# Kernel tuning notes

Hardware: AMD Instinct MI355X
Metric: run time of the kernel (lower is better)

## Reference

```python
import jax, jax.numpy as jnp
import numpy as np

N_ACTIVE = 32

def setup_inputs() -> dict:
    key = jax.random.key(0)
    ks = jax.random.split(key, 6)
    B, T, D, G, GD = 4, 2048, 2048, 4096, 256
    x = jax.random.normal(ks[0], (B, T, D), jnp.float32)
    Wc = jax.random.normal(ks[1], (G, D), jnp.float32) * (D ** -0.5)   # context_proj weight
    temperature = jnp.array(1.0, jnp.float32)
    genes = jax.random.normal(ks[2], (G, GD), jnp.float32) * 0.02      # dna_bank gene table
    Wd = jax.random.normal(ks[3], (D, GD), jnp.float32) * (GD ** -0.5) # gene_to_down weight
    Wu = jax.random.normal(ks[4], (D, GD), jnp.float32) * 0.02         # gene_to_up (zeros in init; random for testing)
    norm_w = jnp.ones((D,), jnp.float32)                               # RMSNorm weight
    scale = jnp.array(0.1, jnp.float32)
    return {"x": x, "Wc": Wc, "temperature": temperature, "genes": genes,
            "Wd": Wd, "Wu": Wu, "norm_w": norm_w, "scale": scale}

def reference(x, Wc, temperature, genes, Wd, Wu, norm_w, scale):
    # RMSNorm (torch default eps = finfo(dtype).eps, learnable elementwise weight)
    eps = jnp.finfo(x.dtype).eps
    xn = x * jax.lax.rsqrt(jnp.mean(x * x, axis=-1, keepdims=True) + eps) * norm_w
    # Expression: router logits over gene bank, temperature clamped at 0.1
    logits = jnp.einsum('btd,gd->btg', xn, Wc) / jnp.clip(temperature, 0.1)
    # top-k + scatter(-inf) + softmax == softmax over top-k values, zeros elsewhere
    top_vals, top_idx = jax.lax.top_k(logits, N_ACTIVE)        # (B,T,K)
    expr_w = jax.nn.softmax(top_vals, axis=-1)                 # (B,T,K)
    # dna_bank.express: weighted combination of genes. Only top-k entries are
    # nonzero, so gather + weighted sum is mathematically identical to the
    # dense (B,T,G)@(G,GD) combine the original materializes.
    expressed = jnp.einsum('btk,btkc->btc', expr_w, genes[top_idx])  # (B,T,GD)
    down = jnp.tanh(jnp.einsum('btc,dc->btd', expressed, Wd))
    up = jnp.einsum('btc,dc->btd', expressed, Wu)
    return down * xn * up * scale
```

## Files before the change

### kernel.cpp

```cpp
#include <hip/hip_runtime.h>
#include <math.h>

#define M_TOK 8192
#define D_DIM 2048
#define G_GENES 4096
#define GD_DIM 256
#define KSEL 32
#define NCAND 40
#define NSLICE 8

typedef float f32x4 __attribute__((ext_vector_type(4)));
typedef short bf16x8 __attribute__((ext_vector_type(8)));

__device__ __forceinline__ void async_copy16(const void* g, void* lds) {
  __builtin_amdgcn_global_load_lds((const __attribute__((address_space(1))) void*)g,
                                   (__attribute__((address_space(3))) void*)lds, 16, 0, 0);
}

__device__ __forceinline__ unsigned short f2bf(float f) {
  unsigned int u = __float_as_uint(f);
  unsigned int r = (u + 0x7fffu + ((u >> 16) & 1u)) >> 16;
  return (unsigned short)r;
}
__device__ __forceinline__ float bf2f(unsigned short h) {
  return __uint_as_float(((unsigned int)h) << 16);
}

__global__ __launch_bounds__(256) void k1_rmsnorm(const float* __restrict__ x,
                                                  const float* __restrict__ nw,
                                                  float* __restrict__ r_out,
                                                  unsigned short* __restrict__ xn_bf) {
  int t = blockIdx.x, tid = threadIdx.x;
  const float4* xr = (const float4*)(x + (size_t)t * D_DIM);
  float4 a = xr[tid], b = xr[tid + 256];
  double ss = (double)a.x*a.x + (double)a.y*a.y + (double)a.z*a.z + (double)a.w*a.w
            + (double)b.x*b.x + (double)b.y*b.y + (double)b.z*b.z + (double)b.w*b.w;
  for (int off = 32; off; off >>= 1) ss += __shfl_down(ss, off);
  __shared__ double sred[4];
  __shared__ float rshare;
  int lane = tid & 63, wv = tid >> 6;
  if (lane == 0) sred[wv] = ss;
  __syncthreads();
  if (tid == 0) {
    double tot = sred[0] + sred[1] + sred[2] + sred[3];
    float r = (float)(1.0 / sqrt(tot / (double)D_DIM + 1.1920928955078125e-7));
    rshare = r; r_out[t] = r;
  }
  __syncthreads();
  float r = rshare;
  const float4* nw4 = (const float4*)nw;
  float4 na = nw4[tid], nb = nw4[tid + 256];
  ushort4 oa, ob;
  oa.x = f2bf(a.x * r * na.x); oa.y = f2bf(a.y * r * na.y);
  oa.z = f2bf(a.z * r * na.z); oa.w = f2bf(a.w * r * na.w);
  ob.x = f2bf(b.x * r * nb.x); ob.y = f2bf(b.y * r * nb.y);
  ob.z = f2bf(b.z * r * nb.z); ob.w = f2bf(b.w * r * nb.w);
  ushort4* o4 = (ushort4*)(xn_bf + (size_t)t * D_DIM);
  o4[tid] = oa; o4[tid + 256] = ob;
}

__global__ __launch_bounds__(256) void k2_cvt(const float* __restrict__ w,
                                              unsigned short* __restrict__ wb) {
  size_t i = (size_t)blockIdx.x * 256 + threadIdx.x;
  const float4* w4 = (const float4*)w;
  float4 a = w4[2*i], b = w4[2*i+1];
  ushort4 oa, ob;
  oa.x = f2bf(a.x); oa.y = f2bf(a.y); oa.z = f2bf(a.z); oa.w = f2bf(a.w);
  ob.x = f2bf(b.x); ob.y = f2bf(b.y); ob.z = f2bf(b.z); ob.w = f2bf(b.w);
  ((ushort4*)wb)[2*i] = oa; ((ushort4*)wb)[2*i+1] = ob;
}

__global__ __launch_bounds__(256) void k2b_split(const float* __restrict__ wd,
                                                 const float* __restrict__ wu,
                                                 unsigned short* __restrict__ wdh,
                                                 unsigned short* __restrict__ wdl,
                                                 unsigned short* __restrict__ wuh,
                                                 unsigned short* __restrict__ wul) {
  const float* src = blockIdx.y ? wu : wd;
  unsigned short* dh = blockIdx.y ? wuh : wdh;
  unsigned short* dl = blockIdx.y ? wul : wdl;
  size_t i = (size_t)blockIdx.x * 256 + threadIdx.x;
  float4 v = ((const float4*)src)[i];
  ushort4 h, l;
  h.x = f2bf(v.x); l.x = f2bf(v.x - bf2f(h.x));
  h.y = f2bf(v.y); l.y = f2bf(v.y - bf2f(h.y));
  h.z = f2bf(v.z); l.z = f2bf(v.z - bf2f(h.z));
  h.w = f2bf(v.w); l.w = f2bf(v.w - bf2f(h.w));
  ((ushort4*)dh)[i] = h;
  ((ushort4*)dl)[i] = l;
}

__global__ __launch_bounds__(512, 1) void k3_gemm_logits(const unsigned short* __restrict__ A,
                                                         const unsigned short* __restrict__ B,
                                                         unsigned short* __restrict__ C) {
  __shared__ unsigned short As[4][256 * 32];
  __shared__ unsigned short Bs[4][256 * 32];
  const int tid = threadIdx.x;
  const int lane = tid & 63, wv = tid >> 6;
  const int wm = wv >> 2, wn = wv & 3;
  int lin = blockIdx.x;
  int swz = (lin & 7) * 64 + (lin >> 3);
  const int bm = swz & 31, bn = swz >> 5;

  const int grow = lane >> 2;
  const int gslot = (lane & 3) ^ ((lane >> 3) & 3);
  const unsigned short* agp = A + (size_t)(bm * 256 + wv * 32 + grow) * D_DIM + gslot * 8;
  const unsigned short* bgp = B + (size_t)(bn * 256 + wv * 32 + grow) * D_DIM + gslot * 8;
  const int fr = lane & 15;
  const int sw8 = (((lane >> 4) ^ ((lane >> 1) & 3))) * 8;

  f32x4 acc[8][4];
#pragma unroll
  for (int m = 0; m < 8; ++m)
#pragma unroll
    for (int n = 0; n < 4; ++n) acc[m][n] = (f32x4){0.f, 0.f, 0.f, 0.f};

#define STAGE_A3(t_) { const int b_ = (t_) & 3; const int kt_ = (t_) * 32;          \
    async_copy16(agp + kt_,              &As[b_][(wv * 32) * 32]);                   \
    async_copy16(agp + kt_ + 16 * D_DIM, &As[b_][(wv * 32 + 16) * 32]); }
#define STAGE_B3(t_) { const int b_ = (t_) & 3; const int kt_ = (t_) * 32;          \
    async_copy16(bgp + kt_,              &Bs[b_][(wv * 32) * 32]);                   \
    async_copy16(bgp + kt_ + 16 * D_DIM, &Bs[b_][(wv * 32 + 16) * 32]); }

  STAGE_A3(0); STAGE_B3(0);
  STAGE_A3(1); STAGE_B3(1);
  STAGE_A3(2); STAGE_B3(2);
  asm volatile("s_waitcnt vmcnt(8)" ::: "memory");
  __builtin_amdgcn_s_barrier();

#pragma unroll 1
  for (int t = 0; t < 64; ++t) {
    const int c = t & 3;
    const unsigned short* as = As[c];
    const unsigned short* bs = Bs[c];
    bf16x8 fa[4], fb[4];
#pragma unroll
    for (int n = 0; n < 4; ++n)
      fb[n] = *(const bf16x8*)&bs[(wn * 64 + n * 16 + fr) * 32 + sw8];
#pragma unroll
    for (int m = 0; m < 4; ++m)
      fa[m] = *(const bf16x8*)&as[(wm * 128 + m * 16 + fr) * 32 + sw8];
    if (t + 3 < 64) STAGE_A3(t + 3);
    __builtin_amdgcn_s_barrier();
    asm volatile("s_waitcnt lgkmcnt(0)" ::: "memory");
    __builtin_amdgcn_sched_barrier(0);
    __builtin_amdgcn_s_setprio(1);
#pragma unroll
    for (int m = 0; m < 4; ++m)
#pragma unroll
      for (int n = 0; n < 4; ++n)
        acc[m][n] = __builtin_amdgcn_mfma_f32_16x16x32_bf16(fa[m], fb[n], acc[m][n], 0, 0, 0);
    __builtin_amdgcn_s_setprio(0);
    __builtin_amdgcn_s_barrier();
#pragma unroll
    for (int m = 0; m < 4; ++m)
      fa[m] = *(const bf16x8*)&as[(wm * 128 + 64 + m * 16 + fr) * 32 + sw8];
    if (t + 3 < 64) STAGE_B3(t + 3);
    __builtin_amdgcn_s_barrier();
    asm volatile("s_waitcnt lgkmcnt(0)" ::: "memory");
    __builtin_amdgcn_sched_barrier(0);
    __builtin_amdgcn_s_setprio(1);
#pragma unroll
    for (int m = 0; m < 4; ++m)
#pragma unroll
      for (int n = 0; n < 4; ++n)
        acc[m + 4][n] = __builtin_amdgcn_mfma_f32_16x16x32_bf16(fa[m], fb[n], acc[m + 4][n], 0, 0, 0);
    __builtin_amdgcn_s_setprio(0);
    if (t <= 60)      { asm volatile("s_waitcnt vmcnt(8)" ::: "memory"); }
    else if (t == 61) { asm volatile("s_waitcnt vmcnt(4)" ::: "memory"); }
    else if (t == 62) { asm volatile("s_waitcnt vmcnt(0)" ::: "memory"); }
    __builtin_amdgcn_s_barrier();
  }
#undef STAGE_A3
#undef STAGE_B3

#pragma unroll
  for (int m = 0; m < 8; ++m)
#pragma unroll
    for (int n = 0; n < 4; ++n)
#pragma unroll
      for (int j = 0; j < 4; ++j) {
        int row = bm * 256 + wm * 128 + m * 16 + (lane >> 4) * 4 + j;
        int col = bn * 256 + wn * 64 + n * 16 + fr;
        C[(size_t)row * G_GENES + col] = f2bf(acc[m][n][j]);
      }
}

__global__ __launch_bounds__(256) void k4_topk(const unsigned short* __restrict__ L,
                                               int* __restrict__ cand) {
  int wv = threadIdx.x >> 6, lane = threadIdx.x & 63;
  int t = blockIdx.x * 4 + wv;
  const unsigned short* lp = L + (size_t)t * G_GENES;
  unsigned kp[32];
#pragma unroll
  for (int i = 0; i < 8; ++i) {
    uint4 raw = *(const uint4*)(lp + i * 512 + lane * 8);
    unsigned rr[4] = {raw.x, raw.y, raw.z, raw.w};
#pragma unroll
    for (int q = 0; q < 4; ++q) {
      unsigned r = rr[q];
      unsigned s = (r >> 15) & 0x00010001u;
      unsigned xm = 0x80008000u | (s * 0x7FFFu);
      kp[i * 4 + q] = r ^ xm;
    }
  }
  unsigned lo = 0, hi = 65536;
  while (hi - lo > 1u) {
    unsigned mid = (lo + hi) >> 1;
    int c = 0;
#pragma unroll
    for (int q = 0; q < 32; ++q) {
      c += __popcll(__ballot((kp[q] & 0xFFFFu) >= mid));
      c += __popcll(__ballot((kp[q] >> 16) >= mid));
    }
    if (c >= NCAND) lo = mid; else hi = mid;
  }
  const unsigned T = lo;
  unsigned long long below = (1ull << lane) - 1ull;
  int* outp = cand + (size_t)t * NCAND;
  int cnt = 0;
#pragma unroll
  for (int q = 0; q < 32; ++q) {
#pragma unroll
    for (int h = 0; h < 2; ++h) {
      unsigned key = h ? (kp[q] >> 16) : (kp[q] & 0xFFFFu);
      bool pred = key > T;
      unsigned long long m = __ballot(pred);
      if (pred) {
        int pos = cnt + (int)__popcll(m & below);
        outp[pos] = (q >> 2) * 512 + lane * 8 + (q & 3) * 2 + h;
      }
      cnt += (int)__popcll(m);
    }
  }
#pragma unroll 1
  for (int q = 0; q < 32 && cnt < NCAND; ++q) {
#pragma unroll
    for (int h = 0; h < 2; ++h) {
      unsigned key = h ? (kp[q] >> 16) : (kp[q] & 0xFFFFu);
      bool pred = key == T;
      unsigned long long m = __ballot(pred);
      if (pred) {
        int pos = cnt + (int)__popcll(m & below);
        if (pos < NCAND)
          outp[pos] = (q >> 2) * 512 + lane * 8 + (q & 3) * 2 + h;
      }
      cnt += (int)__popcll(m);
    }
  }
}

__global__ __launch_bounds__(256) void k5a_partial(const float* __restrict__ x,
                                                   const float* __restrict__ r,
                                                   const float* __restrict__ nw,
                                                   const float* __restrict__ Wc,
                                                   const int* __restrict__ cand,
                                                   double* __restrict__ part) {
  int bid = blockIdx.x;
  int slice = bid & 7;
  int group = bid >> 3;
  int wv = threadIdx.x >> 6, lane = threadIdx.x & 63;
  const int dbase = slice * 256;
  float4 nv = *(const float4*)(nw + dbase + lane * 4);
  bool b0 = (lane & 1) != 0, b1 = (lane & 2) != 0, b2 = (lane & 4) != 0;
#pragma unroll 1
  for (int tt = 0; tt < 2; ++tt) {
    int t = group * 8 + wv * 2 + tt;
    float rr = r[t];
    float4 xv = *(const float4*)(x + (size_t)t * D_DIM + dbase + lane * 4);
    float4 xl;
    xl.x = xv.x * rr * nv.x;
    xl.y = xv.y * rr * nv.y;
    xl.z = xv.z * rr * nv.z;
    xl.w = xv.w * rr * nv.w;
    int myg = cand[t * NCAND + (lane < NCAND ? lane : 0)];
    double* outp = part + ((size_t)t * NSLICE + slice) * NCAND;
#pragma unroll 1
    for (int j0 = 0; j0 < NCAND; j0 += 8) {
      float4 w[8];
#pragma unroll
      for (int c = 0; c < 8; ++c) {
        int g = __shfl(myg, j0 + c);
        w[c] = *(const float4*)(Wc + (size_t)g * D_DIM + dbase + lane * 4);
      }
      double s[8];
#pragma unroll
      for (int c = 0; c < 8; ++c)
        s[c] = ((double)xl.x * (double)w[c].x + (double)xl.y * (double)w[c].y)
             + ((double)xl.z * (double)w[c].z + (double)xl.w * (double)w[c].w);
      double u01 = b0 ? s[1] : s[0], t01 = b0 ? s[0] : s[1];
      double u23 = b0 ? s[3] : s[2], t23 = b0 ? s[2] : s[3];
      double u45 = b0 ? s[5] : s[4], t45 = b0 ? s[4] : s[5];
      double u67 = b0 ? s[7] : s[6], t67 = b0 ? s[6] : s[7];
      u01 += __shfl_xor(t01, 1);
      u23 += __shfl_xor(t23, 1);
      u45 += __shfl_xor(t45, 1);
      u67 += __shfl_xor(t67, 1);
      double v03 = b1 ? u23 : u01, t03 = b1 ? u01 : u23;
      double v47 = b1 ? u67 : u45, t47 = b1 ? u45 : u67;
      v03 += __shfl_xor(t03, 2);
      v47 += __shfl_xor(t47, 2);
      double wsum = b2 ? v47 : v03, t07 = b2 ? v03 : v47;
      wsum += __shfl_xor(t07, 4);
      wsum += __shfl_xor(wsum, 8);
      wsum += __shfl_xor(wsum, 16);
      wsum += __shfl_xor(wsum, 32);
      if (lane < 8) outp[j0 + lane] = wsum;
    }
  }
}

__global__ __launch_bounds__(256) void k6_express(const double* __restrict__ part,
                                                  const int* __restrict__ cand,
                                                  const float* __restrict__ genes,
                                                  const float* __restrict__ temp,
                                                  unsigned short* __restrict__ e_hi,
                                                  unsigned short* __restrict__ e_lo) {
  int t = blockIdx.x, tid = threadIdx.x;
  __shared__ double sval[NCAND];
  __shared__ int sidx[NCAND];
  __shared__ float sw[NCAND];
  float tclamp = fmaxf(temp[0], 0.1f);
  if (tid < NCAND) {
    const double* pp = part + (size_t)t * NSLICE * NCAND + tid;
    double v = 0.0;
#pragma unroll
    for (int s = 0; s < NSLICE; ++s) v += pp[s * NCAND];
    sval[tid] = v / (double)tclamp;
    sidx[tid] = cand[(size_t)t * NCAND + tid];
  }
  __syncthreads();
  if (tid < 64) {
    double v = (tid < NCAND) ? sval[tid] : -1.0e300;
    int gi = (tid < NCAND) ? sidx[tid] : 0x7fffffff;
    int rank = 0;
    for (int j = 0; j < NCAND; ++j) {
      double vj = sval[j]; int gj = sidx[j];
      if (vj > v || (vj == v && gj < gi)) rank++;
    }
    bool sel = (tid < NCAND) && (rank < KSEL);
    double vs = sel ? v : -1.0e300;
    double mx = vs;
    for (int off = 32; off; off >>= 1) { double o = __shfl_xor(mx, off); mx = fmax(mx, o); }
    double e = sel ? exp(v - mx) : 0.0;
    double ssum = e;
    for (int off = 32; off; off >>= 1) ssum += __shfl_xor(ssum, off);
    if (tid < NCAND) sw[tid] = (float)(e / ssum);
  }
  __syncthreads();
  float a0 = 0.f, a1 = 0.f, a2 = 0.f, a3 = 0.f;
#pragma unroll
  for (int k = 0; k < NCAND; k += 4) {
    a0 += sw[k]     * genes[(size_t)sidx[k]     * GD_DIM + tid];
    a1 += sw[k + 1] * genes[(size_t)sidx[k + 1] * GD_DIM + tid];
    a2 += sw[k + 2] * genes[(size_t)sidx[k + 2] * GD_DIM + tid];
    a3 += sw[k + 3] * genes[(size_t)sidx[k + 3] * GD_DIM + tid];
  }
  float acc = (a0 + a1) + (a2 + a3);
  unsigned short h = f2bf(acc);
  unsigned short l = f2bf(acc - bf2f(h));
  e_hi[(size_t)t * GD_DIM + tid] = h;
  e_lo[(size_t)t * GD_DIM + tid] = l;
}

__global__ __launch_bounds__(512, 1) void k7_mfma(const unsigned short* __restrict__ e_hi,
                                                  const unsigned short* __restrict__ e_lo,
                                                  const unsigned short* __restrict__ wdh,
                                                  const unsigned short* __restrict__ wdl,
                                                  const unsigned short* __restrict__ wuh,
                                                  const unsigned short* __restrict__ wul,
                                                  const float* __restrict__ x,
                                                  const float* __restrict__ r,
                                                  const float* __restrict__ nw,
                                                  const float* __restrict__ scale_p,
                                                  float* __restrict__ out) {
  __shared__ unsigned short L[3][6][128 * 32];
  const int tid = threadIdx.x;
  const int lane = tid & 63, wv = tid >> 6;
  const int wm = wv >> 2, wn = wv & 3;
  int lin = blockIdx.x;
  int swz = (lin & 7) * 128 + (lin >> 3);
  const int bm = swz & 63, bn = swz >> 6;

  const int grow = lane >> 2;
  const int gslot = (lane & 3) ^ ((lane >> 3) & 3);
  const int goff = gslot * 8;
  const unsigned short* ehp = e_hi + (size_t)(bm * 128 + wv * 16 + grow) * GD_DIM + goff;
  const unsigned short* elp = e_lo + (size_t)(bm * 128 + wv * 16 + grow) * GD_DIM + goff;
  const unsigned short* dhp = wdh + (size_t)(bn * 128 + wv * 16 + grow) * GD_DIM + goff;
  const unsigned short* dlp = wdl + (size_t)(bn * 128 + wv * 16 + grow) * GD_DIM + goff;
  const unsigned short* uhp = wuh + (size_t)(bn * 128 + wv * 16 + grow) * GD_DIM + goff;
  const unsigned short* ulp = wul + (size_t)(bn * 128 + wv * 16 + grow) * GD_DIM + goff;
  const int ldst = (wv * 16) * 32;

  const int fr = lane & 15;
  const int sw8 = ((lane >> 4) ^ ((lane >> 1) & 3)) * 8;

  f32x4 accD[4][2], accU[4][2];
#pragma unroll
  for (int m = 0; m < 4; ++m)
#pragma unroll
    for (int n = 0; n < 2; ++n) {
      accD[m][n] = (f32x4){0.f, 0.f, 0.f, 0.f};
      accU[m][n] = (f32x4){0.f, 0.f, 0.f, 0.f};
    }

#define STAGE7(t_) if ((t_) < 8) { const int b_ = (t_) % 3; const int kt_ = (t_) * 32; \
    async_copy16(ehp + kt_, &L[b_][0][ldst]); \
    async_copy16(elp + kt_, &L[b_][1][ldst]); \
    async_copy16(dhp + kt_, &L[b_][2][ldst]); \
    async_copy16(dlp + kt_, &L[b_][3][ldst]); \
    async_copy16(uhp + kt_, &L[b_][4][ldst]); \
    async_copy16(ulp + kt_, &L[b_][5][ldst]); }

  STAGE7(0); STAGE7(1);
  asm volatile("s_waitcnt vmcnt(6)" ::: "memory");
  __builtin_amdgcn_s_barrier();

#pragma unroll 1
  for (int t = 0; t < 8; ++t) {
    const int b = t % 3;
    bf16x8 fah[4], fal[4], fh[2], fl[2];
#pragma unroll
    for (int m = 0; m < 4; ++m) {
      int off = (wm * 64 + m * 16 + fr) * 32 + sw8;
      fah[m] = *(const bf16x8*)&L[b][0][off];
      fal[m] = *(const bf16x8*)&L[b][1][off];
    }
#pragma unroll
    for (int n = 0; n < 2; ++n) {
      int off = (wn * 32 + n * 16 + fr) * 32 + sw8;
      fh[n] = *(const bf16x8*)&L[b][2][off];
      fl[n] = *(const bf16x8*)&L[b][3][off];
    }
    STAGE7(t + 2);
    __builtin_amdgcn_s_barrier();
    asm volatile("s_waitcnt lgkmcnt(0)" ::: "memory");
    __builtin_amdgcn_sched_barrier(0);
    __builtin_amdgcn_s_setprio(1);
#pragma unroll
    for (int m = 0; m < 4; ++m)
#pragma unroll
      for (int n = 0; n < 2; ++n) {
        accD[m][n] = __builtin_amdgcn_mfma_f32_16x16x32_bf16(fah[m], fh[n], accD[m][n], 0, 0, 0);
        accD[m][n] = __builtin_amdgcn_mfma_f32_16x16x32_bf16(fah[m], fl[n], accD[m][n], 0, 0, 0);
        accD[m][n] = __builtin_amdgcn_mfma_f32_16x16x32_bf16(fal[m], fh[n], accD[m][n], 0, 0, 0);
      }
    __builtin_amdgcn_s_setprio(0);
    __builtin_amdgcn_s_barrier();
#pragma unroll
    for (int n = 0; n < 2; ++n) {
      int off = (wn * 32 + n * 16 + fr) * 32 + sw8;
      fh[n] = *(const bf16x8*)&L[b][4][off];
      fl[n] = *(const bf16x8*)&L[b][5][off];
    }
    __builtin_amdgcn_s_barrier();
    asm volatile("s_waitcnt lgkmcnt(0)" ::: "memory");
    __builtin_amdgcn_sched_barrier(0);
    __builtin_amdgcn_s_setprio(1);
#pragma unroll
    for (int m = 0; m < 4; ++m)
#pragma unroll
      for (int n = 0; n < 2; ++n) {
        accU[m][n] = __builtin_amdgcn_mfma_f32_16x16x32_bf16(fah[m], fh[n], accU[m][n], 0, 0, 0);
        accU[m][n] = __builtin_amdgcn_mfma_f32_16x16x32_bf16(fah[m], fl[n], accU[m][n], 0, 0, 0);
        accU[m][n] = __builtin_amdgcn_mfma_f32_16x16x32_bf16(fal[m], fh[n], accU[m][n], 0, 0, 0);
      }
    __builtin_amdgcn_s_setprio(0);
    if (t <= 5)      { asm volatile("s_waitcnt vmcnt(6)" ::: "memory"); }
    else if (t == 6) { asm volatile("s_waitcnt vmcnt(0)" ::: "memory"); }
    __builtin_amdgcn_s_barrier();
  }
#undef STAGE7

  float sc = scale_p[0];
#pragma unroll
  for (int m = 0; m < 4; ++m)
#pragma unroll
    for (int j = 0; j < 4; ++j) {
      int token = bm * 128 + wm * 64 + m * 16 + (lane >> 4) * 4 + j;
      float rr = r[token];
#pragma unroll
      for (int n = 0; n < 2; ++n) {
        int d = bn * 128 + wn * 32 + n * 16 + fr;
        float xn = x[(size_t)token * D_DIM + d] * rr * nw[d];
        out[(size_t)token * D_DIM + d] = tanhf(accD[m][n][j]) * xn * accU[m][n][j] * sc;
      }
    }
}

extern "C" void kernel_launch(void* const* d_in, const int* in_sizes, int n_in,
                              void* d_out, int out_size, void* d_ws, size_t ws_size,
                              hipStream_t stream) {
  const float* x       = (const float*)d_in[0];
  const float* Wc      = (const float*)d_in[1];
  const float* temp    = (const float*)d_in[2];
  const float* genes   = (const float*)d_in[3];
  const float* Wd      = (const float*)d_in[4];
  const float* Wu      = (const float*)d_in[5];
  const float* nw      = (const float*)d_in[6];
  const float* scale_p = (const float*)d_in[7];

  char* ws = (char*)d_ws;
  float* r_buf          = (float*)ws;
  unsigned short* xn_bf = (unsigned short*)(ws + 65536);
  unsigned short* wc_bf = (unsigned short*)(ws + 65536 + (size_t)M_TOK * D_DIM * 2);
  char* p = ws + 65536 + (size_t)M_TOK * D_DIM * 2 + (size_t)G_GENES * D_DIM * 2;
  int* cand    = (int*)p;                       p += (size_t)M_TOK * NCAND * 4;
  p += (size_t)M_TOK * NCAND * 8;
  unsigned short* e_hi = (unsigned short*)p;    p += (size_t)M_TOK * GD_DIM * 2;
  unsigned short* e_lo = (unsigned short*)p;

  unsigned short* wdh = (unsigned short*)(ws + 65536);
  unsigned short* wdl = wdh + (size_t)D_DIM * GD_DIM;
  unsigned short* wuh = wdl + (size_t)D_DIM * GD_DIM;
  unsigned short* wul = wuh + (size_t)D_DIM * GD_DIM;
  double* part = (double*)(ws + 65536 + 4ull * D_DIM * GD_DIM * 2);

  unsigned short* logits_bf = (unsigned short*)d_out;

  k1_rmsnorm<<<dim3(M_TOK), dim3(256), 0, stream>>>(x, nw, r_buf, xn_bf);
  k2_cvt<<<dim3((G_GENES * D_DIM) / (256 * 8)), dim3(256), 0, stream>>>(Wc, wc_bf);
  k3_gemm_logits<<<dim3((M_TOK / 256) * (G_GENES / 256)), dim3(512), 0, stream>>>(xn_bf, wc_bf, logits_bf);
  k4_topk<<<dim3(M_TOK / 4), dim3(256), 0, stream>>>(logits_bf, cand);
  k2b_split<<<dim3((D_DIM * GD_DIM) / (256 * 4), 2), dim3(256), 0, stream>>>(Wd, Wu, wdh, wdl, wuh, wul);
  k5a_partial<<<dim3(M_TOK), dim3(256), 0, stream>>>(x, r_buf, nw, Wc, cand, part);
  k6_express<<<dim3(M_TOK), dim3(256), 0, stream>>>(part, cand, genes, temp, e_hi, e_lo);
  k7_mfma<<<dim3((M_TOK / 128) * (D_DIM / 128)), dim3(512), 0, stream>>>(e_hi, e_lo, wdh, wdl, wuh, wul,
                                                                         x, r_buf, nw, scale_p, (float*)d_out);
}
```

Before: 453.8 us.

## Double-buffer LDS fragments in registers and collapse GEMM loop barriers

Restructures the bf16 MFMA logits GEMM main loop so the LDS fragments for the next k-tile are read into a second register set while the MFMAs for the current tile execute. Barriers per iteration drop from four to one, and A/B global staging is issued together with adjusted vmcnt waits. This aims to hide LDS read latency and cut synchronisation stalls, at the cost of more live VGPRs for the two fragment sets, which may pressure occupancy.

```diff
diff --git a/kernel.cpp b/kernel.cpp
--- a/kernel.cpp
+++ b/kernel.cpp
@@ -122,55 +122,56 @@
     async_copy16(bgp + kt_,              &Bs[b_][(wv * 32) * 32]);                   \
     async_copy16(bgp + kt_ + 16 * D_DIM, &Bs[b_][(wv * 32 + 16) * 32]); }
 
+#define READ_FRAGS(fa_, fb_, c_) {                                                   \
+    const unsigned short* as_ = As[c_];                                              \
+    const unsigned short* bs_ = Bs[c_];                                              \
+    _Pragma("unroll") for (int n = 0; n < 4; ++n)                                    \
+      fb_[n] = *(const bf16x8*)&bs_[(wn * 64 + n * 16 + fr) * 32 + sw8];             \
+    _Pragma("unroll") for (int m = 0; m < 8; ++m)                                    \
+      fa_[m] = *(const bf16x8*)&as_[(wm * 128 + m * 16 + fr) * 32 + sw8]; }
+
+#define DO_MFMA(fa_, fb_) {                                                          \
+    _Pragma("unroll") for (int m = 0; m < 4; ++m)                                    \
+      _Pragma("unroll") for (int n = 0; n < 4; ++n)                                  \
+        acc[m][n] = __builtin_amdgcn_mfma_f32_16x16x32_bf16(fa_[m], fb_[n], acc[m][n], 0, 0, 0); \
+    _Pragma("unroll") for (int m = 0; m < 4; ++m)                                    \
+      _Pragma("unroll") for (int n = 0; n < 4; ++n)                                  \
+        acc[m + 4][n] = __builtin_amdgcn_mfma_f32_16x16x32_bf16(fa_[m + 4], fb_[n], acc[m + 4][n], 0, 0, 0); }
+
+#define BODY(t_, CFA, CFB, NFA, NFB) {                                               \
+    if ((t_) + 3 < 64) { STAGE_A3((t_) + 3); STAGE_B3((t_) + 3); }                   \
+    READ_FRAGS(NFA, NFB, ((t_) + 1) & 3);                                            \
+    asm volatile("s_waitcnt lgkmcnt(12)" ::: "memory");                              \
+    __builtin_amdgcn_sched_barrier(0);                                               \
+    __builtin_amdgcn_s_setprio(1);                                                   \
+    DO_MFMA(CFA, CFB);                                                               \
+    __builtin_amdgcn_s_setprio(0);                                                   \
+    if ((t_) <= 60)      { asm volatile("s_waitcnt vmcnt(4)" ::: "memory"); }        \
+    else if ((t_) == 61) { asm volatile("s_waitcnt vmcnt(0)" ::: "memory"); }        \
+    __builtin_amdgcn_s_barrier(); }
+
   STAGE_A3(0); STAGE_B3(0);
   STAGE_A3(1); STAGE_B3(1);
   STAGE_A3(2); STAGE_B3(2);
-  asm volatile("s_waitcnt vmcnt(8)" ::: "memory");
+  asm volatile("s_waitcnt vmcnt(4)" ::: "memory");
   __builtin_amdgcn_s_barrier();
 
+  bf16x8 faA[8], fbA[4], faB[8], fbB[4];
+  READ_FRAGS(faA, fbA, 0);
+
 #pragma unroll 1
-  for (int t = 0; t < 64; ++t) {
-    const int c = t & 3;
-    const unsigned short* as = As[c];
-    const unsigned short* bs = Bs[c];
-    bf16x8 fa[4], fb[4];
-#pragma unroll
-    for (int n = 0; n < 4; ++n)
-      fb[n] = *(const bf16x8*)&bs[(wn * 64 + n * 16 + fr) * 32 + sw8];
-#pragma unroll
-    for (int m = 0; m < 4; ++m)
-      fa[m] = *(const bf16x8*)&as[(wm * 128 + m * 16 + fr) * 32 + sw8];
-    if (t + 3 < 64) STAGE_A3(t + 3);
-    __builtin_amdgcn_s_barrier();
-    asm volatile("s_waitcnt lgkmcnt(0)" ::: "memory");
-    __builtin_amdgcn_sched_barrier(0);
-    __builtin_amdgcn_s_setprio(1);
-#pragma unroll
-    for (int m = 0; m < 4; ++m)
-#pragma unroll
-      for (int n = 0; n < 4; ++n)
-        acc[m][n] = __builtin_amdgcn_mfma_f32_16x16x32_bf16(fa[m], fb[n], acc[m][n], 0, 0, 0);
-    __builtin_amdgcn_s_setprio(0);
-    __builtin_amdgcn_s_barrier();
-#pragma unroll
-    for (int m = 0; m < 4; ++m)
-      fa[m] = *(const bf16x8*)&as[(wm * 128 + 64 + m * 16 + fr) * 32 + sw8];
-    if (t + 3 < 64) STAGE_B3(t + 3);
-    __builtin_amdgcn_s_barrier();
-    asm volatile("s_waitcnt lgkmcnt(0)" ::: "memory");
-    __builtin_amdgcn_sched_barrier(0);
-    __builtin_amdgcn_s_setprio(1);
-#pragma unroll
-    for (int m = 0; m < 4; ++m)
-#pragma unroll
-      for (int n = 0; n < 4; ++n)
-        acc[m + 4][n] = __builtin_amdgcn_mfma_f32_16x16x32_bf16(fa[m], fb[n], acc[m + 4][n], 0, 0, 0);
-    __builtin_amdgcn_s_setprio(0);
-    if (t <= 60)      { asm volatile("s_waitcnt vmcnt(8)" ::: "memory"); }
-    else if (t == 61) { asm volatile("s_waitcnt vmcnt(4)" ::: "memory"); }
-    else if (t == 62) { asm volatile("s_waitcnt vmcnt(0)" ::: "memory"); }
-    __builtin_amdgcn_s_barrier();
-  }
+  for (int t = 0; t < 62; t += 2) {
+    BODY(t,     faA, fbA, faB, fbB);
+    BODY(t + 1, faB, fbB, faA, fbA);
+  }
+  BODY(62, faA, fbA, faB, fbB);
+  asm volatile("s_waitcnt lgkmcnt(0)" ::: "memory");
+  __builtin_amdgcn_sched_barrier(0);
+  DO_MFMA(faB, fbB);
+
+#undef BODY
+#undef DO_MFMA
+#undef READ_FRAGS
 #undef STAGE_A3
 #undef STAGE_B3
 
```

After: 490.0 us. 1.08x slower.
